# Kernel optimization log

Hardware: AMD Instinct MI355X
Metric: run time of the kernel (lower is better)

## Reference

```python
import jax, jax.numpy as jnp
import numpy as np

GAMMA = 0.99
LAM = 0.95
CLIP = 0.2
VALUE_COEFF = 0.5
ENTROPY_COEFF = 0.01
T = 500_000
S = 128
A = 16


def _mlp(x, W1, b1, W2, b2, W3, b3):
    h = jax.nn.relu(x @ W1 + b1)
    h = jax.nn.relu(h @ W2 + b2)
    return h @ W3 + b3


def setup_inputs() -> dict:
    key = jax.random.key(0)
    ks = jax.random.split(key, 12)
    states = jax.random.normal(ks[0], (T, S), dtype=jnp.float32)
    next_states = jax.random.normal(ks[1], (T, S), dtype=jnp.float32)
    rewards = jax.random.normal(ks[2], (T,), dtype=jnp.float32)
    dones = (jax.random.uniform(ks[3], (T,)) < 0.01).astype(jnp.float32)
    actions = jax.random.randint(ks[4], (T,), 0, A)
    # old log-probs of taken actions (valid log-probabilities)
    old_logp = jnp.log(jax.random.uniform(ks[5], (T,), minval=1e-3, maxval=1.0))

    def lin(k, fan_in, fan_out):
        lim = 1.0 / np.sqrt(fan_in)
        return jax.random.uniform(k, (fan_in, fan_out), minval=-lim, maxval=lim, dtype=jnp.float32)

    return {
        'states': states, 'next_states': next_states, 'rewards': rewards,
        'dones': dones, 'actions': actions, 'old_logp': old_logp,
        'aW1': lin(ks[6], S, 64), 'ab1': jnp.zeros((64,), jnp.float32),
        'aW2': lin(ks[7], 64, 64), 'ab2': jnp.zeros((64,), jnp.float32),
        'aW3': lin(ks[8], 64, A), 'ab3': jnp.zeros((A,), jnp.float32),
        'cW1': lin(ks[9], S, 64), 'cb1': jnp.zeros((64,), jnp.float32),
        'cW2': lin(ks[10], 64, 64), 'cb2': jnp.zeros((64,), jnp.float32),
        'cW3': lin(ks[11], 64, 1), 'cb3': jnp.zeros((1,), jnp.float32),
    }


def reference(states, next_states, rewards, dones, actions, old_logp,
              aW1, ab1, aW2, ab2, aW3, ab3,
              cW1, cb1, cW2, cb2, cW3, cb3):
    # ---- critic values and TD deltas ----
    values = _mlp(states, cW1, cb1, cW2, cb2, cW3, cb3)[:, 0]        # [T]
    next_values = _mlp(next_states, cW1, cb1, cW2, cb2, cW3, cb3)[:, 0]
    not_done = 1.0 - dones
    deltas = rewards + GAMMA * next_values * not_done - values       # [T]

    # ---- GAE: reverse-time linear recurrence a_t = c_t * a_{t+1} + d_t ----
    coef = GAMMA * LAM * not_done

    def step(carry, cd):
        c, d = cd
        a = c * carry + d
        return a, a

    _, advantages = jax.lax.scan(step, jnp.float32(0.0), (coef, deltas), reverse=True)
    returns = advantages + values
    adv_n = (advantages - advantages.mean()) / (jnp.std(advantages, ddof=1) + 1e-8)

    # ---- actor: clipped surrogate ----
    probs = jax.nn.softmax(_mlp(states, aW1, ab1, aW2, ab2, aW3, ab3), axis=-1)  # [T, A]
    logp = jnp.log(jnp.take_along_axis(probs, actions[:, None], axis=1))[:, 0]   # [T]
    ratios = jnp.exp(logp - old_logp)
    surr1 = ratios * adv_n
    surr2 = jnp.clip(ratios, 1.0 - CLIP, 1.0 + CLIP) * adv_n
    actor_loss = -jnp.minimum(surr1, surr2).mean()

    # ---- critic MSE loss ----
    critic_loss = jnp.mean((values - returns) ** 2)

    # ---- entropy bonus ----
    entropy_loss = jnp.mean(-jnp.sum(probs * jnp.log(probs + 1e-8), axis=-1))

    total_loss = actor_loss + VALUE_COEFF * critic_loss - ENTROPY_COEFF * entropy_loss
    return jnp.stack([total_loss, actor_loss, critic_loss, entropy_loss])
```

## Files before the change

kernel.cpp:

```cpp
#include <hip/hip_runtime.h>

#define T_N 500000
#define NTILE 31250
#define NCHUNK 4096
#define CHUNKL 128
#define NPART 1024

typedef __attribute__((ext_vector_type(8))) short short8v;
typedef __attribute__((ext_vector_type(4))) float float4v;

__device__ __forceinline__ short f2bf(float f) {
    union { float f; unsigned u; } v; v.f = f;
    unsigned r = v.u + 0x7FFFu + ((v.u >> 16) & 1u);
    return (short)(r >> 16);
}

#define FC1 0
#define FA1 16
#define FC2 32
#define FA2 40
#define FA3 48
#define NFRAG 50

__global__ __launch_bounds__(64) void k_pack(
    const float* __restrict__ cW1, const float* __restrict__ aW1,
    const float* __restrict__ cW2, const float* __restrict__ aW2,
    const float* __restrict__ aW3, short8v* __restrict__ packed)
{
    const int f = blockIdx.x, l = threadIdx.x;
    const int g = l >> 4, col = l & 15;
    const float* W; int s, c, ncol;
    if (f < FA1)      { W = cW1; s = f >> 2;         c = f & 3;         ncol = 64; }
    else if (f < FC2) { W = aW1; s = (f - FA1) >> 2; c = (f - FA1) & 3; ncol = 64; }
    else if (f < FA2) { W = cW2; s = (f - FC2) >> 2; c = (f - FC2) & 3; ncol = 64; }
    else if (f < FA3) { W = aW2; s = (f - FA2) >> 2; c = (f - FA2) & 3; ncol = 64; }
    else              { W = aW3; s = f - FA3;        c = 0;             ncol = 16; }
    short8v frag;
    #pragma unroll
    for (int j = 0; j < 8; ++j) {
        int k = s * 32 + g * 8 + j;
        frag[j] = f2bf(W[k * ncol + c * 16 + col]);
    }
    packed[f * 64 + l] = frag;
}

__global__ __launch_bounds__(256) void k_mlp(
    const float* __restrict__ states, const float* __restrict__ next_states,
    const float* __restrict__ rewards, const float* __restrict__ dones,
    const int* __restrict__ actions, const float* __restrict__ old_logp,
    const short8v* __restrict__ pk,
    const float* __restrict__ cb1, const float* __restrict__ ab1,
    const float* __restrict__ cb2, const float* __restrict__ ab2,
    const float* __restrict__ ab3,
    const float* __restrict__ cW3, const float* __restrict__ cb3,
    float* __restrict__ delta_o, float* __restrict__ coef_o,
    float* __restrict__ ratio_o, float* __restrict__ ent_o)
{
    __shared__ __align__(16) short hlds[4][16][72];
    const int wv = threadIdx.x >> 6, l = threadIdx.x & 63;
    const int g = l >> 4, q = l & 15;
    const long long tile = (long long)blockIdx.x * 4 + wv;
    if (tile >= NTILE) return;
    const long long r0 = tile * 16;
    short (*h)[72] = hlds[wv];

    float4v accC[4], accA[4];
    #pragma unroll
    for (int c = 0; c < 4; ++c) {
        float b = cb1[c * 16 + q];  accC[c] = (float4v){b, b, b, b};
        float b2 = ab1[c * 16 + q]; accA[c] = (float4v){b2, b2, b2, b2};
    }
    {
        const float* xs = states + (r0 + q) * 128;
        #pragma unroll
        for (int s = 0; s < 4; ++s) {
            float4 xa = *reinterpret_cast<const float4*>(xs + s * 32 + g * 8);
            float4 xb = *reinterpret_cast<const float4*>(xs + s * 32 + g * 8 + 4);
            short8v af;
            af[0] = f2bf(xa.x); af[1] = f2bf(xa.y); af[2] = f2bf(xa.z); af[3] = f2bf(xa.w);
            af[4] = f2bf(xb.x); af[5] = f2bf(xb.y); af[6] = f2bf(xb.z); af[7] = f2bf(xb.w);
            #pragma unroll
            for (int c = 0; c < 4; ++c) {
                accC[c] = __builtin_amdgcn_mfma_f32_16x16x32_bf16(af, pk[(FC1 + s * 4 + c) * 64 + l], accC[c], 0, 0, 0);
                accA[c] = __builtin_amdgcn_mfma_f32_16x16x32_bf16(af, pk[(FA1 + s * 4 + c) * 64 + l], accA[c], 0, 0, 0);
            }
        }
    }

    #pragma unroll
    for (int c = 0; c < 4; ++c)
        #pragma unroll
        for (int r = 0; r < 4; ++r)
            h[g * 4 + r][c * 16 + q] = f2bf(fmaxf(accC[c][r], 0.f));
    float4v acc2[4];
    #pragma unroll
    for (int c = 0; c < 4; ++c) { float b = cb2[c * 16 + q]; acc2[c] = (float4v){b, b, b, b}; }
    #pragma unroll
    for (int s = 0; s < 2; ++s) {
        short8v a2 = *reinterpret_cast<const short8v*>(&h[q][s * 32 + g * 8]);
        #pragma unroll
        for (int c = 0; c < 4; ++c)
            acc2[c] = __builtin_amdgcn_mfma_f32_16x16x32_bf16(a2, pk[(FC2 + s * 4 + c) * 64 + l], acc2[c], 0, 0, 0);
    }
    float vr[4] = {0.f, 0.f, 0.f, 0.f};
    #pragma unroll
    for (int c = 0; c < 4; ++c) {
        float w = cW3[c * 16 + q];
        #pragma unroll
        for (int r = 0; r < 4; ++r) vr[r] = fmaf(fmaxf(acc2[c][r], 0.f), w, vr[r]);
    }
    #pragma unroll
    for (int o = 1; o < 16; o <<= 1)
        #pragma unroll
        for (int r = 0; r < 4; ++r) vr[r] += __shfl_xor(vr[r], o);
    const float cb3v = cb3[0];
    float v[4];
    #pragma unroll
    for (int r = 0; r < 4; ++r) v[r] = vr[r] + cb3v;

    #pragma unroll
    for (int c = 0; c < 4; ++c)
        #pragma unroll
        for (int r = 0; r < 4; ++r)
            h[g * 4 + r][c * 16 + q] = f2bf(fmaxf(accA[c][r], 0.f));
    float4v acc2a[4];
    #pragma unroll
    for (int c = 0; c < 4; ++c) { float b = ab2[c * 16 + q]; acc2a[c] = (float4v){b, b, b, b}; }
    #pragma unroll
    for (int s = 0; s < 2; ++s) {
        short8v a2 = *reinterpret_cast<const short8v*>(&h[q][s * 32 + g * 8]);
        #pragma unroll
        for (int c = 0; c < 4; ++c)
            acc2a[c] = __builtin_amdgcn_mfma_f32_16x16x32_bf16(a2, pk[(FA2 + s * 4 + c) * 64 + l], acc2a[c], 0, 0, 0);
    }
    #pragma unroll
    for (int c = 0; c < 4; ++c)
        #pragma unroll
        for (int r = 0; r < 4; ++r)
            h[g * 4 + r][c * 16 + q] = f2bf(fmaxf(acc2a[c][r], 0.f));
    const float b3 = ab3[q];
    float4v acc3 = (float4v){b3, b3, b3, b3};
    #pragma unroll
    for (int s = 0; s < 2; ++s) {
        short8v a3 = *reinterpret_cast<const short8v*>(&h[q][s * 32 + g * 8]);
        acc3 = __builtin_amdgcn_mfma_f32_16x16x32_bf16(a3, pk[(FA3 + s) * 64 + l], acc3, 0, 0, 0);
    }
    float lg[4], mx[4], pe[4], se[4], entv[4], sl[4], logp[4];
    #pragma unroll
    for (int r = 0; r < 4; ++r) { lg[r] = acc3[r]; mx[r] = lg[r]; }
    #pragma unroll
    for (int o = 1; o < 16; o <<= 1)
        #pragma unroll
        for (int r = 0; r < 4; ++r) mx[r] = fmaxf(mx[r], __shfl_xor(mx[r], o));
    #pragma unroll
    for (int r = 0; r < 4; ++r) { pe[r] = expf(lg[r] - mx[r]); se[r] = pe[r]; }
    #pragma unroll
    for (int o = 1; o < 16; o <<= 1)
        #pragma unroll
        for (int r = 0; r < 4; ++r) se[r] += __shfl_xor(se[r], o);
    #pragma unroll
    for (int r = 0; r < 4; ++r) { float pr = pe[r] / se[r]; entv[r] = -pr * logf(pr + 1e-8f); }
    #pragma unroll
    for (int o = 1; o < 16; o <<= 1)
        #pragma unroll
        for (int r = 0; r < 4; ++r) entv[r] += __shfl_xor(entv[r], o);
    const int4 av = *reinterpret_cast<const int4*>(&actions[r0 + g * 4]);
    const int act[4] = {av.x, av.y, av.z, av.w};
    #pragma unroll
    for (int r = 0; r < 4; ++r) sl[r] = (q == act[r]) ? lg[r] : -3.0e38f;
    #pragma unroll
    for (int o = 1; o < 16; o <<= 1)
        #pragma unroll
        for (int r = 0; r < 4; ++r) sl[r] = fmaxf(sl[r], __shfl_xor(sl[r], o));
    #pragma unroll
    for (int r = 0; r < 4; ++r) logp[r] = sl[r] - mx[r] - logf(se[r]);

    float4v accN[4];
    #pragma unroll
    for (int c = 0; c < 4; ++c) { float b = cb1[c * 16 + q]; accN[c] = (float4v){b, b, b, b}; }
    {
        const float* xn = next_states + (r0 + q) * 128;
        #pragma unroll
        for (int s = 0; s < 4; ++s) {
            float4 xa = *reinterpret_cast<const float4*>(xn + s * 32 + g * 8);
            float4 xb = *reinterpret_cast<const float4*>(xn + s * 32 + g * 8 + 4);
            short8v af;
            af[0] = f2bf(xa.x); af[1] = f2bf(xa.y); af[2] = f2bf(xa.z); af[3] = f2bf(xa.w);
            af[4] = f2bf(xb.x); af[5] = f2bf(xb.y); af[6] = f2bf(xb.z); af[7] = f2bf(xb.w);
            #pragma unroll
            for (int c = 0; c < 4; ++c)
                accN[c] = __builtin_amdgcn_mfma_f32_16x16x32_bf16(af, pk[(FC1 + s * 4 + c) * 64 + l], accN[c], 0, 0, 0);
        }
    }
    #pragma unroll
    for (int c = 0; c < 4; ++c)
        #pragma unroll
        for (int r = 0; r < 4; ++r)
            h[g * 4 + r][c * 16 + q] = f2bf(fmaxf(accN[c][r], 0.f));
    float4v acc2n[4];
    #pragma unroll
    for (int c = 0; c < 4; ++c) { float b = cb2[c * 16 + q]; acc2n[c] = (float4v){b, b, b, b}; }
    #pragma unroll
    for (int s = 0; s < 2; ++s) {
        short8v a2 = *reinterpret_cast<const short8v*>(&h[q][s * 32 + g * 8]);
        #pragma unroll
        for (int c = 0; c < 4; ++c)
            acc2n[c] = __builtin_amdgcn_mfma_f32_16x16x32_bf16(a2, pk[(FC2 + s * 4 + c) * 64 + l], acc2n[c], 0, 0, 0);
    }
    float nr[4] = {0.f, 0.f, 0.f, 0.f};
    #pragma unroll
    for (int c = 0; c < 4; ++c) {
        float w = cW3[c * 16 + q];
        #pragma unroll
        for (int r = 0; r < 4; ++r) nr[r] = fmaf(fmaxf(acc2n[c][r], 0.f), w, nr[r]);
    }
    #pragma unroll
    for (int o = 1; o < 16; o <<= 1)
        #pragma unroll
        for (int r = 0; r < 4; ++r) nr[r] += __shfl_xor(nr[r], o);
    float nv[4];
    #pragma unroll
    for (int r = 0; r < 4; ++r) nv[r] = nr[r] + cb3v;

    if (q == 0) {
        const long long rb = r0 + g * 4;
        const float4 rw = *reinterpret_cast<const float4*>(&rewards[rb]);
        const float4 dn = *reinterpret_cast<const float4*>(&dones[rb]);
        const float4 ol = *reinterpret_cast<const float4*>(&old_logp[rb]);
        const float rwv[4] = {rw.x, rw.y, rw.z, rw.w};
        const float dnv[4] = {dn.x, dn.y, dn.z, dn.w};
        const float olv[4] = {ol.x, ol.y, ol.z, ol.w};
        float dl[4], cf[4], rt[4];
        const float GL = (float)(0.99 * 0.95);
        #pragma unroll
        for (int r = 0; r < 4; ++r) {
            float nd = 1.f - dnv[r];
            dl[r] = fmaf(0.99f * nd, nv[r], rwv[r]) - v[r];
            cf[r] = GL * nd;
            rt[r] = expf(logp[r] - olv[r]);
        }
        float4 t;
        t.x = dl[0]; t.y = dl[1]; t.z = dl[2]; t.w = dl[3];
        *reinterpret_cast<float4*>(&delta_o[rb]) = t;
        t.x = cf[0]; t.y = cf[1]; t.z = cf[2]; t.w = cf[3];
        *reinterpret_cast<float4*>(&coef_o[rb]) = t;
        t.x = rt[0]; t.y = rt[1]; t.z = rt[2]; t.w = rt[3];
        *reinterpret_cast<float4*>(&ratio_o[rb]) = t;
        t.x = entv[0]; t.y = entv[1]; t.z = entv[2]; t.w = entv[3];
        *reinterpret_cast<float4*>(&ent_o[rb]) = t;
    }
}

__global__ __launch_bounds__(256) void k_gae_chunk(
    const float* __restrict__ coef, const float* __restrict__ delta,
    float* __restrict__ P, float* __restrict__ Q)
{
    const int c = blockIdx.x * 256 + threadIdx.x;
    const long long lo = (long long)c * CHUNKL;
    float p = 1.f, a = 0.f;
    if (lo < T_N) {
        const int n = (int)((T_N - lo < CHUNKL) ? (T_N - lo) : CHUNKL);
        for (int j = (n >> 2) - 1; j >= 0; --j) {
            float4 cfv = *reinterpret_cast<const float4*>(&coef[lo + 4 * j]);
            float4 dlv = *reinterpret_cast<const float4*>(&delta[lo + 4 * j]);
            a = fmaf(cfv.w, a, dlv.w);
            a = fmaf(cfv.z, a, dlv.z);
            a = fmaf(cfv.y, a, dlv.y);
            a = fmaf(cfv.x, a, dlv.x);
            p *= cfv.x * cfv.y * cfv.z * cfv.w;
        }
    }
    P[c] = p; Q[c] = a;
}

__global__ __launch_bounds__(1024) void k_gae_scan(
    const float* __restrict__ P, const float* __restrict__ Q,
    float* __restrict__ carry)
{
    __shared__ float sp[1024], sq[1024];
    const int t = threadIdx.x, b = t * 4;
    float p = P[b + 3], q = Q[b + 3];
    #pragma unroll
    for (int c = 2; c >= 0; --c) {
        float pc = P[b + c], qc = Q[b + c];
        q = fmaf(pc, q, qc);
        p = pc * p;
    }
    sp[t] = p; sq[t] = q;
    __syncthreads();
    for (int d = 1; d < 1024; d <<= 1) {
        float pp = sp[t], qq = sq[t];
        float p2 = 1.f, q2 = 0.f;
        const bool has = (t + d) < 1024;
        if (has) { p2 = sp[t + d]; q2 = sq[t + d]; }
        __syncthreads();
        if (has) { sp[t] = pp * p2; sq[t] = fmaf(pp, q2, qq); }
        __syncthreads();
    }
    float x = (t + 1 < 1024) ? sq[t + 1] : 0.f;
    #pragma unroll
    for (int c = 3; c >= 0; --c) {
        carry[b + c] = x;
        x = fmaf(P[b + c], x, Q[b + c]);
    }
}

__global__ __launch_bounds__(256) void k_gae_apply(
    const float* __restrict__ coef, const float* __restrict__ delta,
    const float* __restrict__ carry, float* __restrict__ adv,
    float* __restrict__ part)
{
    const int c = blockIdx.x * 256 + threadIdx.x;
    const long long lo = (long long)c * CHUNKL;
    float s = 0.f, s2 = 0.f;
    if (lo < T_N) {
        const int n = (int)((T_N - lo < CHUNKL) ? (T_N - lo) : CHUNKL);
        float a = carry[c];
        for (int j = (n >> 2) - 1; j >= 0; --j) {
            float4 cfv = *reinterpret_cast<const float4*>(&coef[lo + 4 * j]);
            float4 dlv = *reinterpret_cast<const float4*>(&delta[lo + 4 * j]);
            float a3 = fmaf(cfv.w, a, dlv.w);
            float a2v = fmaf(cfv.z, a3, dlv.z);
            float a1 = fmaf(cfv.y, a2v, dlv.y);
            float a0 = fmaf(cfv.x, a1, dlv.x);
            float4 o; o.x = a0; o.y = a1; o.z = a2v; o.w = a3;
            *reinterpret_cast<float4*>(&adv[lo + 4 * j]) = o;
            a = a0;
            s += a0 + a1 + a2v + a3;
            s2 += a0 * a0 + a1 * a1 + a2v * a2v + a3 * a3;
        }
    }
    #pragma unroll
    for (int o = 32; o > 0; o >>= 1) { s += __shfl_down(s, o); s2 += __shfl_down(s2, o); }
    __shared__ float l0[4], l1[4];
    const int wv = threadIdx.x >> 6, ln = threadIdx.x & 63;
    if (ln == 0) { l0[wv] = s; l1[wv] = s2; }
    __syncthreads();
    if (threadIdx.x == 0) {
        part[blockIdx.x * 2]     = l0[0] + l0[1] + l0[2] + l0[3];
        part[blockIdx.x * 2 + 1] = l1[0] + l1[1] + l1[2] + l1[3];
    }
}

__global__ __launch_bounds__(256) void k_actor(
    const float* __restrict__ adv, const float* __restrict__ ratio,
    const float* __restrict__ ent, const float* __restrict__ part,
    float* __restrict__ part4)
{
    __shared__ float st[2];
    if (threadIdx.x == 0) {
        float S = 0.f, S2 = 0.f;
        #pragma unroll
        for (int i = 0; i < 16; ++i) { S += part[2 * i]; S2 += part[2 * i + 1]; }
        const float Tf = (float)T_N;
        float mean = S / Tf;
        float var = (S2 - S * S / Tf) / (Tf - 1.f);
        st[0] = mean;
        st[1] = 1.f / (sqrtf(fmaxf(var, 0.f)) + 1e-8f);
    }
    __syncthreads();
    const float mean = st[0], isd = st[1];
    float sm = 0.f, se = 0.f;
    for (long long i = (long long)blockIdx.x * 256 + threadIdx.x; i < T_N;
         i += (long long)gridDim.x * 256) {
        float an = (adv[i] - mean) * isd;
        float rt = ratio[i];
        float s1 = rt * an;
        float s2v = fminf(fmaxf(rt, 0.8f), 1.2f) * an;
        sm += fminf(s1, s2v);
        se += ent[i];
    }
    #pragma unroll
    for (int o = 32; o > 0; o >>= 1) { sm += __shfl_down(sm, o); se += __shfl_down(se, o); }
    __shared__ float l0[4], l1[4];
    const int wv = threadIdx.x >> 6, ln = threadIdx.x & 63;
    if (ln == 0) { l0[wv] = sm; l1[wv] = se; }
    __syncthreads();
    if (threadIdx.x == 0) {
        part4[blockIdx.x * 2]     = l0[0] + l0[1] + l0[2] + l0[3];
        part4[blockIdx.x * 2 + 1] = l1[0] + l1[1] + l1[2] + l1[3];
    }
}

__global__ __launch_bounds__(1024) void k_final(
    const float* __restrict__ part4, const float* __restrict__ part,
    float* __restrict__ out)
{
    const int t = threadIdx.x;
    float sm = part4[t * 2], se = part4[t * 2 + 1];
    #pragma unroll
    for (int o = 32; o > 0; o >>= 1) { sm += __shfl_down(sm, o); se += __shfl_down(se, o); }
    __shared__ float l0[16], l1[16];
    const int wv = t >> 6, ln = t & 63;
    if (ln == 0) { l0[wv] = sm; l1[wv] = se; }
    __syncthreads();
    if (t == 0) {
        float SM = 0.f, SE = 0.f;
        #pragma unroll
        for (int i = 0; i < 16; ++i) { SM += l0[i]; SE += l1[i]; }
        float S2 = 0.f;
        #pragma unroll
        for (int i = 0; i < 16; ++i) S2 += part[2 * i + 1];
        const float Tf = (float)T_N;
        float actor_loss = -SM / Tf;
        float ent_loss = SE / Tf;
        float critic_loss = S2 / Tf;
        float total = actor_loss + 0.5f * critic_loss - 0.01f * ent_loss;
        out[0] = total; out[1] = actor_loss; out[2] = critic_loss; out[3] = ent_loss;
    }
}

extern "C" void kernel_launch(void* const* d_in, const int* in_sizes, int n_in,
                              void* d_out, int out_size, void* d_ws, size_t ws_size,
                              hipStream_t stream) {
    (void)in_sizes; (void)n_in; (void)out_size; (void)ws_size;
    const float* states      = (const float*)d_in[0];
    const float* next_states = (const float*)d_in[1];
    const float* rewards     = (const float*)d_in[2];
    const float* dones       = (const float*)d_in[3];
    const int*   actions     = (const int*)d_in[4];
    const float* old_logp    = (const float*)d_in[5];
    const float* aW1 = (const float*)d_in[6];  const float* ab1 = (const float*)d_in[7];
    const float* aW2 = (const float*)d_in[8];  const float* ab2 = (const float*)d_in[9];
    const float* aW3 = (const float*)d_in[10]; const float* ab3 = (const float*)d_in[11];
    const float* cW1 = (const float*)d_in[12]; const float* cb1 = (const float*)d_in[13];
    const float* cW2 = (const float*)d_in[14]; const float* cb2 = (const float*)d_in[15];
    const float* cW3 = (const float*)d_in[16]; const float* cb3 = (const float*)d_in[17];
    float* out = (float*)d_out;

    float* ws = (float*)d_ws;
    float* delta = ws;
    float* coef  = ws + 1 * (size_t)T_N;
    float* ratio = ws + 2 * (size_t)T_N;
    float* entb  = ws + 3 * (size_t)T_N;
    float* adv   = ws + 4 * (size_t)T_N;
    float* P     = ws + 5 * (size_t)T_N;
    float* Q     = P + NCHUNK;
    float* carry = Q + NCHUNK;
    float* part  = carry + NCHUNK;
    float* part4 = part + 32;
    short8v* packed = (short8v*)(part4 + 2048);

    k_pack<<<NFRAG, 64, 0, stream>>>(cW1, aW1, cW2, aW2, aW3, packed);
    k_mlp<<<(NTILE + 3) / 4, 256, 0, stream>>>(
        states, next_states, rewards, dones, actions, old_logp, packed,
        cb1, ab1, cb2, ab2, ab3, cW3, cb3, delta, coef, ratio, entb);
    k_gae_chunk<<<NCHUNK / 256, 256, 0, stream>>>(coef, delta, P, Q);
    k_gae_scan<<<1, 1024, 0, stream>>>(P, Q, carry);
    k_gae_apply<<<NCHUNK / 256, 256, 0, stream>>>(coef, delta, carry, adv, part);
    k_actor<<<NPART, 256, 0, stream>>>(adv, ratio, entb, part, part4);
    k_final<<<1, 1024, 0, stream>>>(part4, part, out);
}
```

Measured before the change: 224.6 us.

## Process 32 rows per wave and keep weight fragments in registers across layers

Each wave now handles two 16-row tiles, with every layer's packed bf16 weight fragments loaded into registers once and reused for both tiles and for the states and next_states passes. The critic is run on all four tiles before the actor, using four LDS activation buffers with a 68-short row pitch. The float-to-bf16 conversion now uses the HIP intrinsic. The aim is fewer repeated weight loads and more MFMA work per wave, at the cost of higher register pressure (lower occupancy) and half as many waves to hide the memory-bound state loads.

```diff
diff --git a/kernel.cpp b/kernel.cpp
--- a/kernel.cpp
+++ b/kernel.cpp
@@ -1,7 +1,8 @@
 #include <hip/hip_runtime.h>
+#include <hip/hip_bf16.h>
 
 #define T_N 500000
-#define NTILE 31250
+#define NTILE2 15625
 #define NCHUNK 4096
 #define CHUNKL 128
 #define NPART 1024
@@ -10,9 +11,8 @@
 typedef __attribute__((ext_vector_type(4))) float float4v;
 
 __device__ __forceinline__ short f2bf(float f) {
-    union { float f; unsigned u; } v; v.f = f;
-    unsigned r = v.u + 0x7FFFu + ((v.u >> 16) & 1u);
-    return (short)(r >> 16);
+    __hip_bfloat16 b = __float2bfloat16(f);
+    return *reinterpret_cast<short*>(&b);
 }
 
 #define FC1 0
@@ -42,6 +42,105 @@
         frag[j] = f2bf(W[k * ncol + c * 16 + col]);
     }
     packed[f * 64 + l] = frag;
+}
+
+__device__ __forceinline__ short8v pack_afrag(const float* __restrict__ xrow, int off) {
+    float4 xa = *reinterpret_cast<const float4*>(xrow + off);
+    float4 xb = *reinterpret_cast<const float4*>(xrow + off + 4);
+    short8v af;
+    af[0] = f2bf(xa.x); af[1] = f2bf(xa.y); af[2] = f2bf(xa.z); af[3] = f2bf(xa.w);
+    af[4] = f2bf(xb.x); af[5] = f2bf(xb.y); af[6] = f2bf(xb.z); af[7] = f2bf(xb.w);
+    return af;
+}
+
+__device__ __forceinline__ void store_h(short (*hb)[68], const float4v* acc, int g, int q) {
+    #pragma unroll
+    for (int c = 0; c < 4; ++c)
+        #pragma unroll
+        for (int r = 0; r < 4; ++r)
+            hb[g * 4 + r][c * 16 + q] = f2bf(fmaxf(acc[c][r], 0.f));
+}
+
+__device__ __forceinline__ void l2_critic(const short* hbase, const short8v* fc2,
+                                          const float* bc2, const float* w3, float cb3v,
+                                          int g, int q, float* vout)
+{
+    float4v acc[4];
+    #pragma unroll
+    for (int c = 0; c < 4; ++c) acc[c] = (float4v){bc2[c], bc2[c], bc2[c], bc2[c]};
+    #pragma unroll
+    for (int s = 0; s < 2; ++s) {
+        short8v a2 = *reinterpret_cast<const short8v*>(hbase + q * 68 + s * 32 + g * 8);
+        #pragma unroll
+        for (int c = 0; c < 4; ++c)
+            acc[c] = __builtin_amdgcn_mfma_f32_16x16x32_bf16(a2, fc2[s * 4 + c], acc[c], 0, 0, 0);
+    }
+    float vr[4] = {0.f, 0.f, 0.f, 0.f};
+    #pragma unroll
+    for (int c = 0; c < 4; ++c)
+        #pragma unroll
+        for (int r = 0; r < 4; ++r) vr[r] = fmaf(fmaxf(acc[c][r], 0.f), w3[c], vr[r]);
+    #pragma unroll
+    for (int o = 1; o < 16; o <<= 1)
+        #pragma unroll
+        for (int r = 0; r < 4; ++r) vr[r] += __shfl_xor(vr[r], o);
+    #pragma unroll
+    for (int r = 0; r < 4; ++r) vout[r] = vr[r] + cb3v;
+}
+
+__device__ __forceinline__ void actor_head(const short* h_in, short (*h_tmp)[68],
+                                           const short8v* fa2, const short8v* fa3,
+                                           const float* ba2, float ab3q,
+                                           int g, int q, long long r0s,
+                                           const int* __restrict__ actions,
+                                           float* logp, float* entv)
+{
+    float4v acc[4];
+    #pragma unroll
+    for (int c = 0; c < 4; ++c) acc[c] = (float4v){ba2[c], ba2[c], ba2[c], ba2[c]};
+    #pragma unroll
+    for (int s = 0; s < 2; ++s) {
+        short8v a2 = *reinterpret_cast<const short8v*>(h_in + q * 68 + s * 32 + g * 8);
+        #pragma unroll
+        for (int c = 0; c < 4; ++c)
+            acc[c] = __builtin_amdgcn_mfma_f32_16x16x32_bf16(a2, fa2[s * 4 + c], acc[c], 0, 0, 0);
+    }
+    store_h(h_tmp, acc, g, q);
+    float4v acc3 = (float4v){ab3q, ab3q, ab3q, ab3q};
+    #pragma unroll
+    for (int s = 0; s < 2; ++s) {
+        short8v a3 = *reinterpret_cast<const short8v*>(&h_tmp[q][s * 32 + g * 8]);
+        acc3 = __builtin_amdgcn_mfma_f32_16x16x32_bf16(a3, fa3[s], acc3, 0, 0, 0);
+    }
+    float lg[4], mx[4], pe[4], se[4], sl[4];
+    #pragma unroll
+    for (int r = 0; r < 4; ++r) { lg[r] = acc3[r]; mx[r] = lg[r]; }
+    #pragma unroll
+    for (int o = 1; o < 16; o <<= 1)
+        #pragma unroll
+        for (int r = 0; r < 4; ++r) mx[r] = fmaxf(mx[r], __shfl_xor(mx[r], o));
+    #pragma unroll
+    for (int r = 0; r < 4; ++r) { pe[r] = expf(lg[r] - mx[r]); se[r] = pe[r]; }
+    #pragma unroll
+    for (int o = 1; o < 16; o <<= 1)
+        #pragma unroll
+        for (int r = 0; r < 4; ++r) se[r] += __shfl_xor(se[r], o);
+    #pragma unroll
+    for (int r = 0; r < 4; ++r) { float pr = pe[r] / se[r]; entv[r] = -pr * logf(pr + 1e-8f); }
+    #pragma unroll
+    for (int o = 1; o < 16; o <<= 1)
+        #pragma unroll
+        for (int r = 0; r < 4; ++r) entv[r] += __shfl_xor(entv[r], o);
+    const int4 av = *reinterpret_cast<const int4*>(&actions[r0s + g * 4]);
+    const int act[4] = {av.x, av.y, av.z, av.w};
+    #pragma unroll
+    for (int r = 0; r < 4; ++r) sl[r] = (q == act[r]) ? lg[r] : -3.0e38f;
+    #pragma unroll
+    for (int o = 1; o < 16; o <<= 1)
+        #pragma unroll
+        for (int r = 0; r < 4; ++r) sl[r] = fmaxf(sl[r], __shfl_xor(sl[r], o));
+    #pragma unroll
+    for (int r = 0; r < 4; ++r) logp[r] = sl[r] - mx[r] - logf(se[r]);
 }
 
 __global__ __launch_bounds__(256) void k_mlp(
@@ -56,198 +155,163 @@
     float* __restrict__ delta_o, float* __restrict__ coef_o,
     float* __restrict__ ratio_o, float* __restrict__ ent_o)
 {
-    __shared__ __align__(16) short hlds[4][16][72];
+    __shared__ __align__(16) short hlds[4][4][16][68];
     const int wv = threadIdx.x >> 6, l = threadIdx.x & 63;
     const int g = l >> 4, q = l & 15;
-    const long long tile = (long long)blockIdx.x * 4 + wv;
-    if (tile >= NTILE) return;
-    const long long r0 = tile * 16;
-    short (*h)[72] = hlds[wv];
-
-    float4v accC[4], accA[4];
-    #pragma unroll
-    for (int c = 0; c < 4; ++c) {
-        float b = cb1[c * 16 + q];  accC[c] = (float4v){b, b, b, b};
-        float b2 = ab1[c * 16 + q]; accA[c] = (float4v){b2, b2, b2, b2};
+    const int tile = blockIdx.x * 4 + wv;
+    if (tile >= NTILE2) return;
+    const long long r0 = (long long)tile * 32;
+    short (*hb0)[68] = hlds[wv][0];
+    short (*hb1)[68] = hlds[wv][1];
+    short (*hb2)[68] = hlds[wv][2];
+    short (*hb3)[68] = hlds[wv][3];
+
+    float bc1[4];
+    #pragma unroll
+    for (int c = 0; c < 4; ++c) bc1[c] = cb1[c * 16 + q];
+    short8v fc1[16];
+    #pragma unroll
+    for (int f = 0; f < 16; ++f) fc1[f] = pk[(FC1 + f) * 64 + l];
+
+    const float* xs0 = states + (r0 + q) * 128;
+    const float* xs1 = xs0 + 16 * 128;
+    short8v sa0[4], sa1[4];
+    #pragma unroll
+    for (int s = 0; s < 4; ++s) {
+        sa0[s] = pack_afrag(xs0, s * 32 + g * 8);
+        sa1[s] = pack_afrag(xs1, s * 32 + g * 8);
     }
     {
-        const float* xs = states + (r0 + q) * 128;
-        #pragma unroll
-        for (int s = 0; s < 4; ++s) {
-            float4 xa = *reinterpret_cast<const float4*>(xs + s * 32 + g * 8);
-            float4 xb = *reinterpret_cast<const float4*>(xs + s * 32 + g * 8 + 4);
-            short8v af;
-            af[0] = f2bf(xa.x); af[1] = f2bf(xa.y); af[2] = f2bf(xa.z); af[3] = f2bf(xa.w);
-            af[4] = f2bf(xb.x); af[5] = f2bf(xb.y); af[6] = f2bf(xb.z); af[7] = f2bf(xb.w);
+        float4v aC0[4], aC1[4];
+        #pragma unroll
+        for (int c = 0; c < 4; ++c) {
+            aC0[c] = (float4v){bc1[c], bc1[c], bc1[c], bc1[c]};
+            aC1[c] = aC0[c];
+        }
+        #pragma unroll
+        for (int s = 0; s < 4; ++s)
             #pragma unroll
             for (int c = 0; c < 4; ++c) {
-                accC[c] = __builtin_amdgcn_mfma_f32_16x16x32_bf16(af, pk[(FC1 + s * 4 + c) * 64 + l], accC[c], 0, 0, 0);
-                accA[c] = __builtin_amdgcn_mfma_f32_16x16x32_bf16(af, pk[(FA1 + s * 4 + c) * 64 + l], accA[c], 0, 0, 0);
+                aC0[c] = __builtin_amdgcn_mfma_f32_16x16x32_bf16(sa0[s], fc1[s * 4 + c], aC0[c], 0, 0, 0);
+                aC1[c] = __builtin_amdgcn_mfma_f32_16x16x32_bf16(sa1[s], fc1[s * 4 + c], aC1[c], 0, 0, 0);
             }
-        }
-    }
-
-    #pragma unroll
-    for (int c = 0; c < 4; ++c)
-        #pragma unroll
-        for (int r = 0; r < 4; ++r)
-            h[g * 4 + r][c * 16 + q] = f2bf(fmaxf(accC[c][r], 0.f));
-    float4v acc2[4];
-    #pragma unroll
-    for (int c = 0; c < 4; ++c) { float b = cb2[c * 16 + q]; acc2[c] = (float4v){b, b, b, b}; }
-    #pragma unroll
-    for (int s = 0; s < 2; ++s) {
-        short8v a2 = *reinterpret_cast<const short8v*>(&h[q][s * 32 + g * 8]);
-        #pragma unroll
-        for (int c = 0; c < 4; ++c)
-            acc2[c] = __builtin_amdgcn_mfma_f32_16x16x32_bf16(a2, pk[(FC2 + s * 4 + c) * 64 + l], acc2[c], 0, 0, 0);
-    }
-    float vr[4] = {0.f, 0.f, 0.f, 0.f};
-    #pragma unroll
-    for (int c = 0; c < 4; ++c) {
-        float w = cW3[c * 16 + q];
-        #pragma unroll
-        for (int r = 0; r < 4; ++r) vr[r] = fmaf(fmaxf(acc2[c][r], 0.f), w, vr[r]);
-    }
-    #pragma unroll
-    for (int o = 1; o < 16; o <<= 1)
-        #pragma unroll
-        for (int r = 0; r < 4; ++r) vr[r] += __shfl_xor(vr[r], o);
-    const float cb3v = cb3[0];
-    float v[4];
-    #pragma unroll
-    for (int r = 0; r < 4; ++r) v[r] = vr[r] + cb3v;
-
-    #pragma unroll
-    for (int c = 0; c < 4; ++c)
-        #pragma unroll
-        for (int r = 0; r < 4; ++r)
-            h[g * 4 + r][c * 16 + q] = f2bf(fmaxf(accA[c][r], 0.f));
-    float4v acc2a[4];
-    #pragma unroll
-    for (int c = 0; c < 4; ++c) { float b = ab2[c * 16 + q]; acc2a[c] = (float4v){b, b, b, b}; }
-    #pragma unroll
-    for (int s = 0; s < 2; ++s) {
-        short8v a2 = *reinterpret_cast<const short8v*>(&h[q][s * 32 + g * 8]);
-        #pragma unroll
-        for (int c = 0; c < 4; ++c)
-            acc2a[c] = __builtin_amdgcn_mfma_f32_16x16x32_bf16(a2, pk[(FA2 + s * 4 + c) * 64 + l], acc2a[c], 0, 0, 0);
-    }
-    #pragma unroll
-    for (int c = 0; c < 4; ++c)
-        #pragma unroll
-        for (int r = 0; r < 4; ++r)
-            h[g * 4 + r][c * 16 + q] = f2bf(fmaxf(acc2a[c][r], 0.f));
-    const float b3 = ab3[q];
-    float4v acc3 = (float4v){b3, b3, b3, b3};
-    #pragma unroll
-    for (int s = 0; s < 2; ++s) {
-        short8v a3 = *reinterpret_cast<const short8v*>(&h[q][s * 32 + g * 8]);
-        acc3 = __builtin_amdgcn_mfma_f32_16x16x32_bf16(a3, pk[(FA3 + s) * 64 + l], acc3, 0, 0, 0);
-    }
-    float lg[4], mx[4], pe[4], se[4], entv[4], sl[4], logp[4];
-    #pragma unroll
-    for (int r = 0; r < 4; ++r) { lg[r] = acc3[r]; mx[r] = lg[r]; }
-    #pragma unroll
-    for (int o = 1; o < 16; o <<= 1)
-        #pragma unroll
-        for (int r = 0; r < 4; ++r) mx[r] = fmaxf(mx[r], __shfl_xor(mx[r], o));
-    #pragma unroll
-    for (int r = 0; r < 4; ++r) { pe[r] = expf(lg[r] - mx[r]); se[r] = pe[r]; }
-    #pragma unroll
-    for (int o = 1; o < 16; o <<= 1)
-        #pragma unroll
-        for (int r = 0; r < 4; ++r) se[r] += __shfl_xor(se[r], o);
-    #pragma unroll
-    for (int r = 0; r < 4; ++r) { float pr = pe[r] / se[r]; entv[r] = -pr * logf(pr + 1e-8f); }
-    #pragma unroll
-    for (int o = 1; o < 16; o <<= 1)
-        #pragma unroll
-        for (int r = 0; r < 4; ++r) entv[r] += __shfl_xor(entv[r], o);
-    const int4 av = *reinterpret_cast<const int4*>(&actions[r0 + g * 4]);
-    const int act[4] = {av.x, av.y, av.z, av.w};
-    #pragma unroll
-    for (int r = 0; r < 4; ++r) sl[r] = (q == act[r]) ? lg[r] : -3.0e38f;
-    #pragma unroll
-    for (int o = 1; o < 16; o <<= 1)
-        #pragma unroll
-        for (int r = 0; r < 4; ++r) sl[r] = fmaxf(sl[r], __shfl_xor(sl[r], o));
-    #pragma unroll
-    for (int r = 0; r < 4; ++r) logp[r] = sl[r] - mx[r] - logf(se[r]);
-
-    float4v accN[4];
-    #pragma unroll
-    for (int c = 0; c < 4; ++c) { float b = cb1[c * 16 + q]; accN[c] = (float4v){b, b, b, b}; }
+        store_h(hb0, aC0, g, q);
+        store_h(hb1, aC1, g, q);
+    }
     {
-        const float* xn = next_states + (r0 + q) * 128;
-        #pragma unroll
-        for (int s = 0; s < 4; ++s) {
-            float4 xa = *reinterpret_cast<const float4*>(xn + s * 32 + g * 8);
-            float4 xb = *reinterpret_cast<const float4*>(xn + s * 32 + g * 8 + 4);
-            short8v af;
-            af[0] = f2bf(xa.x); af[1] = f2bf(xa.y); af[2] = f2bf(xa.z); af[3] = f2bf(xa.w);
-            af[4] = f2bf(xb.x); af[5] = f2bf(xb.y); af[6] = f2bf(xb.z); af[7] = f2bf(xb.w);
+        const float* xn0 = next_states + (r0 + q) * 128;
+        short8v na[4];
+        #pragma unroll
+        for (int s = 0; s < 4; ++s) na[s] = pack_afrag(xn0, s * 32 + g * 8);
+        float4v aN[4];
+        #pragma unroll
+        for (int c = 0; c < 4; ++c) aN[c] = (float4v){bc1[c], bc1[c], bc1[c], bc1[c]};
+        #pragma unroll
+        for (int s = 0; s < 4; ++s)
             #pragma unroll
             for (int c = 0; c < 4; ++c)
-                accN[c] = __builtin_amdgcn_mfma_f32_16x16x32_bf16(af, pk[(FC1 + s * 4 + c) * 64 + l], accN[c], 0, 0, 0);
+                aN[c] = __builtin_amdgcn_mfma_f32_16x16x32_bf16(na[s], fc1[s * 4 + c], aN[c], 0, 0, 0);
+        store_h(hb2, aN, g, q);
+        const float* xn1 = xn0 + 16 * 128;
+        #pragma unroll
+        for (int s = 0; s < 4; ++s) na[s] = pack_afrag(xn1, s * 32 + g * 8);
+        #pragma unroll
+        for (int c = 0; c < 4; ++c) aN[c] = (float4v){bc1[c], bc1[c], bc1[c], bc1[c]};
+        #pragma unroll
+        for (int s = 0; s < 4; ++s)
+            #pragma unroll
+            for (int c = 0; c < 4; ++c)
+                aN[c] = __builtin_amdgcn_mfma_f32_16x16x32_bf16(na[s], fc1[s * 4 + c], aN[c], 0, 0, 0);
+        store_h(hb3, aN, g, q);
+    }
+
+    float v0[4], v1[4], nv0[4], nv1[4];
+    {
+        short8v fc2[8];
+        #pragma unroll
+        for (int f = 0; f < 8; ++f) fc2[f] = pk[(FC2 + f) * 64 + l];
+        float bc2[4], w3[4];
+        #pragma unroll
+        for (int c = 0; c < 4; ++c) { bc2[c] = cb2[c * 16 + q]; w3[c] = cW3[c * 16 + q]; }
+        const float cb3v = cb3[0];
+        l2_critic(&hb0[0][0], fc2, bc2, w3, cb3v, g, q, v0);
+        l2_critic(&hb1[0][0], fc2, bc2, w3, cb3v, g, q, v1);
+        l2_critic(&hb2[0][0], fc2, bc2, w3, cb3v, g, q, nv0);
+        l2_critic(&hb3[0][0], fc2, bc2, w3, cb3v, g, q, nv1);
+    }
+
+    {
+        float ba1[4];
+        #pragma unroll
+        for (int c = 0; c < 4; ++c) ba1[c] = ab1[c * 16 + q];
+        short8v fa1[16];
+        #pragma unroll
+        for (int f = 0; f < 16; ++f) fa1[f] = pk[(FA1 + f) * 64 + l];
+        float4v aA0[4], aA1[4];
+        #pragma unroll
+        for (int c = 0; c < 4; ++c) {
+            aA0[c] = (float4v){ba1[c], ba1[c], ba1[c], ba1[c]};
+            aA1[c] = aA0[c];
         }
-    }
-    #pragma unroll
-    for (int c = 0; c < 4; ++c)
-        #pragma unroll
-        for (int r = 0; r < 4; ++r)
-            h[g * 4 + r][c * 16 + q] = f2bf(fmaxf(accN[c][r], 0.f));
-    float4v acc2n[4];
-    #pragma unroll
-    for (int c = 0; c < 4; ++c) { float b = cb2[c * 16 + q]; acc2n[c] = (float4v){b, b, b, b}; }
-    #pragma unroll
-    for (int s = 0; s < 2; ++s) {
-        short8v a2 = *reinterpret_cast<const short8v*>(&h[q][s * 32 + g * 8]);
-        #pragma unroll
-        for (int c = 0; c < 4; ++c)
-            acc2n[c] = __builtin_amdgcn_mfma_f32_16x16x32_bf16(a2, pk[(FC2 + s * 4 + c) * 64 + l], acc2n[c], 0, 0, 0);
-    }
-    float nr[4] = {0.f, 0.f, 0.f, 0.f};
-    #pragma unroll
-    for (int c = 0; c < 4; ++c) {
-        float w = cW3[c * 16 + q];
-        #pragma unroll
-        for (int r = 0; r < 4; ++r) nr[r] = fmaf(fmaxf(acc2n[c][r], 0.f), w, nr[r]);
-    }
-    #pragma unroll
-    for (int o = 1; o < 16; o <<= 1)
-        #pragma unroll
-        for (int r = 0; r < 4; ++r) nr[r] += __shfl_xor(nr[r], o);
-    float nv[4];
-    #pragma unroll
-    for (int r = 0; r < 4; ++r) nv[r] = nr[r] + cb3v;
+        #pragma unroll
+        for (int s = 0; s < 4; ++s)
+            #pragma unroll
+            for (int c = 0; c < 4; ++c) {
+                aA0[c] = __builtin_amdgcn_mfma_f32_16x16x32_bf16(sa0[s], fa1[s * 4 + c], aA0[c], 0, 0, 0);
+                aA1[c] = __builtin_amdgcn_mfma_f32_16x16x32_bf16(sa1[s], fa1[s * 4 + c], aA1[c], 0, 0, 0);
+            }
+        store_h(hb0, aA0, g, q);
+        store_h(hb1, aA1, g, q);
+    }
+
+    float logp0[4], ent0[4], logp1[4], ent1[4];
+    {
+        short8v fa2[8], fa3[2];
+        #pragma unroll
+        for (int f = 0; f < 8; ++f) fa2[f] = pk[(FA2 + f) * 64 + l];
+        fa3[0] = pk[(FA3 + 0) * 64 + l];
+        fa3[1] = pk[(FA3 + 1) * 64 + l];
+        float ba2[4];
+        #pragma unroll
+        for (int c = 0; c < 4; ++c) ba2[c] = ab2[c * 16 + q];
+        const float ab3q = ab3[q];
+        actor_head(&hb0[0][0], hb2, fa2, fa3, ba2, ab3q, g, q, r0,      actions, logp0, ent0);
+        actor_head(&hb1[0][0], hb3, fa2, fa3, ba2, ab3q, g, q, r0 + 16, actions, logp1, ent1);
+    }
 
     if (q == 0) {
-        const long long rb = r0 + g * 4;
-        const float4 rw = *reinterpret_cast<const float4*>(&rewards[rb]);
-        const float4 dn = *reinterpret_cast<const float4*>(&dones[rb]);
-        const float4 ol = *reinterpret_cast<const float4*>(&old_logp[rb]);
-        const float rwv[4] = {rw.x, rw.y, rw.z, rw.w};
-        const float dnv[4] = {dn.x, dn.y, dn.z, dn.w};
-        const float olv[4] = {ol.x, ol.y, ol.z, ol.w};
-        float dl[4], cf[4], rt[4];
-        const float GL = (float)(0.99 * 0.95);
-        #pragma unroll
-        for (int r = 0; r < 4; ++r) {
-            float nd = 1.f - dnv[r];
-            dl[r] = fmaf(0.99f * nd, nv[r], rwv[r]) - v[r];
-            cf[r] = GL * nd;
-            rt[r] = expf(logp[r] - olv[r]);
+        const float GL = 0.99f * 0.95f;
+        #pragma unroll
+        for (int sub = 0; sub < 2; ++sub) {
+            const long long rb = r0 + sub * 16 + g * 4;
+            const float* vv = sub ? v1 : v0;
+            const float* nn = sub ? nv1 : nv0;
+            const float* lp = sub ? logp1 : logp0;
+            const float* ev = sub ? ent1 : ent0;
+            const float4 rw = *reinterpret_cast<const float4*>(&rewards[rb]);
+            const float4 dn = *reinterpret_cast<const float4*>(&dones[rb]);
+            const float4 ol = *reinterpret_cast<const float4*>(&old_logp[rb]);
+            const float rwv[4] = {rw.x, rw.y, rw.z, rw.w};
+            const float dnv[4] = {dn.x, dn.y, dn.z, dn.w};
+            const float olv[4] = {ol.x, ol.y, ol.z, ol.w};
+            float dl[4], cf[4], rt[4];
+            #pragma unroll
+            for (int r = 0; r < 4; ++r) {
+                float nd = 1.f - dnv[r];
+                dl[r] = fmaf(0.99f * nd, nn[r], rwv[r]) - vv[r];
+                cf[r] = GL * nd;
+                rt[r] = expf(lp[r] - olv[r]);
+            }
+            float4 t;
+            t.x = dl[0]; t.y = dl[1]; t.z = dl[2]; t.w = dl[3];
+            *reinterpret_cast<float4*>(&delta_o[rb]) = t;
+            t.x = cf[0]; t.y = cf[1]; t.z = cf[2]; t.w = cf[3];
+            *reinterpret_cast<float4*>(&coef_o[rb]) = t;
+            t.x = rt[0]; t.y = rt[1]; t.z = rt[2]; t.w = rt[3];
+            *reinterpret_cast<float4*>(&ratio_o[rb]) = t;
+            t.x = ev[0]; t.y = ev[1]; t.z = ev[2]; t.w = ev[3];
+            *reinterpret_cast<float4*>(&ent_o[rb]) = t;
         }
-        float4 t;
-        t.x = dl[0]; t.y = dl[1]; t.z = dl[2]; t.w = dl[3];
-        *reinterpret_cast<float4*>(&delta_o[rb]) = t;
-        t.x = cf[0]; t.y = cf[1]; t.z = cf[2]; t.w = cf[3];
-        *reinterpret_cast<float4*>(&coef_o[rb]) = t;
-        t.x = rt[0]; t.y = rt[1]; t.z = rt[2]; t.w = rt[3];
-        *reinterpret_cast<float4*>(&ratio_o[rb]) = t;
-        t.x = entv[0]; t.y = entv[1]; t.z = entv[2]; t.w = entv[3];
-        *reinterpret_cast<float4*>(&ent_o[rb]) = t;
     }
 }
 
@@ -442,7 +506,7 @@
     short8v* packed = (short8v*)(part4 + 2048);
 
     k_pack<<<NFRAG, 64, 0, stream>>>(cW1, aW1, cW2, aW2, aW3, packed);
-    k_mlp<<<(NTILE + 3) / 4, 256, 0, stream>>>(
+    k_mlp<<<(NTILE2 + 3) / 4, 256, 0, stream>>>(
         states, next_states, rewards, dones, actions, old_logp, packed,
         cb1, ab1, cb2, ab2, ab3, cW3, cb3, delta, coef, ratio, entb);
     k_gae_chunk<<<NCHUNK / 256, 256, 0, stream>>>(coef, delta, P, Q);
```

New measurement: 213.5 us. -4.9%, faster.
